# Optimization experiments

Measured on AMD Instinct MI355X. Metric: run time of the kernel, lower is better.

Reference implementation:

```python
import jax, jax.numpy as jnp
import numpy as np

D_MODEL = 1024
N_HEADS = 16
HEAD_DIM = D_MODEL // N_HEADS  # 64
BASE = 10000.0
MAX_X, MAX_Y, MAX_Z = 32, 32, 8
NEG_INF = -1e9  # stand-in for float('-inf') in masked_fill; identical after softmax


def _split_dims(head_dim):
    n_pairs = head_dim // 2
    px = n_pairs // 3
    py = n_pairs // 3
    pz = n_pairs - px - py
    return px * 2, py * 2, pz * 2


def _cos_sin_table(dim, max_pos):
    # matches RotaryEmbedding3D._register_cache
    inv_freq = 1.0 / (BASE ** (np.arange(0, dim, 2, dtype=np.float32) / dim))
    t = np.arange(max_pos, dtype=np.float32)[:, None] * inv_freq  # [max_pos, dim/2]
    cos = np.repeat(np.cos(t), 2, axis=-1)  # repeat_interleave(2)
    sin = np.repeat(np.sin(t), 2, axis=-1)
    return jnp.asarray(cos), jnp.asarray(sin)


def _rotate_half(x):
    x1 = x[..., ::2]
    x2 = x[..., 1::2]
    return jnp.stack((-x2, x1), axis=-1).reshape(x.shape)


def setup_inputs() -> dict:
    key = jax.random.key(0)
    k1, k2, k3, k4, k5, k6 = jax.random.split(key, 6)
    B, S = 2, 2048
    hidden_states = jax.random.normal(k1, (B, S, D_MODEL), dtype=jnp.float32)
    w_qkv = jax.random.normal(k2, (D_MODEL, 3 * D_MODEL), dtype=jnp.float32) * 0.02
    w_out = jax.random.normal(k3, (D_MODEL, D_MODEL), dtype=jnp.float32) * 0.02
    px = jax.random.randint(k4, (B, S, 1), 0, MAX_X)
    py = jax.random.randint(k5, (B, S, 1), 0, MAX_Y)
    pz = jax.random.randint(k6, (B, S, 1), 0, MAX_Z)
    pos_xyz = jnp.concatenate([px, py, pz], axis=-1).astype(jnp.int64)
    causal_mask = jnp.triu(jnp.ones((S, S), dtype=bool), k=1)[None, None]  # [1,1,S,S]
    return {"hidden_states": hidden_states, "w_qkv": w_qkv, "w_out": w_out,
            "pos_xyz": pos_xyz, "causal_mask": causal_mask}


def reference(hidden_states, w_qkv, w_out, pos_xyz, causal_mask):
    B, S, D = hidden_states.shape
    H, Hd = N_HEADS, HEAD_DIM
    # fused QKV projection
    qkv = hidden_states @ w_qkv  # [B,S,3D]
    qkv = qkv.reshape(B, S, 3, H, Hd).transpose(2, 0, 3, 1, 4)  # [3,B,H,S,Hd]
    q, k, v = qkv[0], qkv[1], qkv[2]
    # 3D RoPE tables and lookups
    dx, dy, dz = _split_dims(Hd)
    cx, sx = _cos_sin_table(dx, MAX_X)
    cy, sy = _cos_sin_table(dy, MAX_Y)
    cz, sz = _cos_sin_table(dz, MAX_Z)
    ix = jnp.clip(pos_xyz[..., 0], 0, MAX_X - 1)
    iy = jnp.clip(pos_xyz[..., 1], 0, MAX_Y - 1)
    iz = jnp.clip(pos_xyz[..., 2], 0, MAX_Z - 1)
    cos = jnp.concatenate([cx[ix], cy[iy], cz[iz]], axis=-1)[:, None]  # [B,1,S,Hd]
    sin = jnp.concatenate([sx[ix], sy[iy], sz[iz]], axis=-1)[:, None]
    q = q * cos + _rotate_half(q) * sin
    k = k * cos + _rotate_half(k) * sin
    # SDPA with causal bias
    scale = Hd ** -0.5
    scores = jnp.einsum('bhqd,bhkd->bhqk', q, k) * scale
    scores = jnp.where(causal_mask, jnp.asarray(NEG_INF, scores.dtype), scores)
    probs = jax.nn.softmax(scores, axis=-1)
    attn = jnp.einsum('bhqk,bhkd->bhqd', probs, v)
    attn = attn.transpose(0, 2, 1, 3).reshape(B, S, D)
    return attn @ w_out
```

## Files before the change

### kernel.cpp

```cpp
#include <hip/hip_runtime.h>
#include <hip/hip_bf16.h>
#include <math.h>

typedef __bf16 bf16;
typedef __bf16 bf16x8 __attribute__((ext_vector_type(8)));
typedef float f32x4 __attribute__((ext_vector_type(4)));

#define SEQ 2048
#define NHEADS 16
#define HDIM 64
#define DM 1024
#define QKVW 3072

__device__ __forceinline__ void gload_lds16(const void* g, void* l) {
  __builtin_amdgcn_global_load_lds(
      (const __attribute__((address_space(1))) unsigned int*)g,
      (__attribute__((address_space(3))) unsigned int*)l, 16, 0, 0);
}

template <int CTRL>
__device__ __forceinline__ float dppmovf(float x) {
  return __builtin_bit_cast(
      float, __builtin_amdgcn_mov_dpp(__builtin_bit_cast(int, x), CTRL, 0xf,
                                      0xf, true));
}
__device__ __forceinline__ float rowsum16(float x) {
  x += dppmovf<0xB1>(x);
  x += dppmovf<0x4E>(x);
  x += dppmovf<0x124>(x);
  x += dppmovf<0x128>(x);
  return x;
}

__global__ __launch_bounds__(256) void prep(
    const float* __restrict__ hidden, const float* __restrict__ w_qkv,
    const float* __restrict__ w_out, const int* __restrict__ pos,
    bf16* __restrict__ hid_bf, bf16* __restrict__ wqkvT,
    bf16* __restrict__ woutT, float2* __restrict__ tbl) {
  __shared__ float tile[64][65];
  int idx = blockIdx.x, tid = threadIdx.x;
  if (idx < 2048) {
    int i = (idx * 256 + tid) * 8;
    float4 a = *(const float4*)(hidden + i);
    float4 b = *(const float4*)(hidden + i + 4);
    bf16x8 o;
    o[0] = (bf16)a.x; o[1] = (bf16)a.y; o[2] = (bf16)a.z; o[3] = (bf16)a.w;
    o[4] = (bf16)b.x; o[5] = (bf16)b.y; o[6] = (bf16)b.z; o[7] = (bf16)b.w;
    *(bf16x8*)(hid_bf + i) = o;
  } else if (idx < 3072) {
    const float* in; bf16* out; int R, C, t;
    if (idx < 2816) { t = idx - 2048; in = w_qkv; out = wqkvT; R = 1024; C = 3072; }
    else            { t = idx - 2816; in = w_out; out = woutT; R = 1024; C = 1024; }
    int nbx = C >> 6;
    int c0 = (t % nbx) * 64, r0 = (t / nbx) * 64;
    int col = tid & 63, rb = (tid >> 6) * 16;
#pragma unroll
    for (int i = 0; i < 16; ++i)
      tile[rb + i][col] = in[(size_t)(r0 + rb + i) * C + c0 + col];
    __syncthreads();
#pragma unroll
    for (int i = 0; i < 16; ++i)
      out[(size_t)(c0 + rb + i) * R + r0 + col] = (bf16)tile[col][rb + i];
  } else {
    const float LN1E4 = 9.210340371976184f;
    int gi = (idx - 3072) * 256 + tid;
    int m = gi >> 5, pr = gi & 31;
    int axis, d, iloc;
    if (pr < 10)      { axis = 0; d = 20; iloc = pr; }
    else if (pr < 20) { axis = 1; d = 20; iloc = pr - 10; }
    else              { axis = 2; d = 24; iloc = pr - 20; }
    int p = pos[m * 3 + axis];
    int pmax = (axis == 2) ? 7 : 31;
    p = p < 0 ? 0 : (p > pmax ? pmax : p);
    float invf = __expf(-((float)(2 * iloc) / (float)d) * LN1E4);
    float sn, cs;
    __sincosf((float)p * invf, &sn, &cs);
    tbl[gi] = make_float2(cs, sn);
  }
}

__global__ __launch_bounds__(256) void post_qkv(
    bf16* __restrict__ qkv, const float2* __restrict__ tbl,
    bf16* __restrict__ vT) {
  __shared__ bf16 btile[64][65];
  int idx = blockIdx.x, tid = threadIdx.x;
  if (idx < 2048) {
    int gi = idx * 256 + tid;
    int m = gi >> 7, seg = gi & 127;
    bf16* p = qkv + (size_t)m * QKVW + seg * 16;
    bf16x8 a = *(const bf16x8*)p;
    bf16x8 b2 = *(const bf16x8*)(p + 8);
    const float2* t = tbl + m * 32 + (((seg * 16) & 63) >> 1);
#pragma unroll
    for (int j = 0; j < 4; ++j) {
      float2 cs = t[j];
      float e = (float)a[2 * j], o = (float)a[2 * j + 1];
      a[2 * j]     = (bf16)(e * cs.x - o * cs.y);
      a[2 * j + 1] = (bf16)(o * cs.x + e * cs.y);
    }
#pragma unroll
    for (int j = 0; j < 4; ++j) {
      float2 cs = t[4 + j];
      float e = (float)b2[2 * j], o = (float)b2[2 * j + 1];
      b2[2 * j]     = (bf16)(e * cs.x - o * cs.y);
      b2[2 * j + 1] = (bf16)(o * cs.x + e * cs.y);
    }
    *(bf16x8*)p = a;
    *(bf16x8*)(p + 8) = b2;
  } else {
    int t = idx - 2048;
    int s0 = (t & 31) * 64, bh = t >> 5;
    int b = bh >> 4, h = bh & 15;
    const bf16* src = qkv + (size_t)(b * SEQ + s0) * QKVW + 2 * DM + h * 64;
    int col = tid & 63, rb = (tid >> 6) * 16;
#pragma unroll
    for (int i = 0; i < 16; ++i)
      btile[rb + i][col] = src[(size_t)(rb + i) * QKVW + col];
    __syncthreads();
    bf16* dst = vT + (size_t)bh * HDIM * SEQ + s0;
#pragma unroll
    for (int i = 0; i < 16; ++i)
      dst[(size_t)(rb + i) * SEQ + col] = btile[col][rb + i];
  }
}

template <int OUTBF>
__global__ __launch_bounds__(256) void gemm_bt(
    const bf16* __restrict__ A, const bf16* __restrict__ Bt, void* Cv,
    int M, int N, int K) {
  __shared__ __align__(16) bf16 a_lds[128 * 32];
  __shared__ __align__(16) bf16 b_lds[128 * 32];
  int tid = threadIdx.x;
  int wave = tid >> 6, lane = tid & 63;
  int quad = lane >> 4, l15 = lane & 15;
  int wm = wave >> 1, wn = wave & 1;

  int flat = blockIdx.y * gridDim.x + blockIdx.x;
  int mband = gridDim.y >> 3;
  int xcd = flat & 7, sidx = flat >> 3;
  int m0 = (xcd * mband + (sidx % mband)) * 128;
  int n0 = (sidx / mband) * 128;

  f32x4 acc[4][4] = {};

  for (int kt = 0; kt < K; kt += 32) {
    __syncthreads();
#pragma unroll
    for (int call = 0; call < 2; ++call) {
      int chunk = call * 256 + tid;
      int row = chunk >> 2, cc = (chunk & 3) * 8;
      gload_lds16(A + (size_t)(m0 + row) * K + kt + cc,
                  (char*)a_lds + call * 4096 + wave * 1024);
      gload_lds16(Bt + (size_t)(n0 + row) * K + kt + cc,
                  (char*)b_lds + call * 4096 + wave * 1024);
    }
    __syncthreads();
    bf16x8 af[4], bfr[4];
#pragma unroll
    for (int i = 0; i < 4; ++i) {
      af[i]  = *(const bf16x8*)(a_lds + (wm * 64 + i * 16 + l15) * 32 + quad * 8);
      bfr[i] = *(const bf16x8*)(b_lds + (wn * 64 + i * 16 + l15) * 32 + quad * 8);
    }
#pragma unroll
    for (int mi = 0; mi < 4; ++mi)
#pragma unroll
      for (int ni = 0; ni < 4; ++ni)
        acc[mi][ni] = __builtin_amdgcn_mfma_f32_16x16x32_bf16(
            af[mi], bfr[ni], acc[mi][ni], 0, 0, 0);
  }

#pragma unroll
  for (int mi = 0; mi < 4; ++mi) {
    int mb = m0 + wm * 64 + mi * 16 + quad * 4;
#pragma unroll
    for (int ni = 0; ni < 4; ++ni) {
      int n = n0 + wn * 64 + ni * 16 + l15;
#pragma unroll
      for (int r = 0; r < 4; ++r) {
        if (OUTBF)
          ((bf16*)Cv)[(size_t)(mb + r) * N + n] = (bf16)acc[mi][ni][r];
        else
          ((float*)Cv)[(size_t)(mb + r) * N + n] = acc[mi][ni][r];
      }
    }
  }
}

__global__ __launch_bounds__(256) void attn_fwd(
    const bf16* __restrict__ QKV, const bf16* __restrict__ VT,
    bf16* __restrict__ O) {
  __shared__ __align__(16) bf16 k_lds[64 * 72];
  __shared__ __align__(16) bf16 v_lds[64 * 72];
  __shared__ __align__(16) bf16 p_lds[4][16 * 80];
  const float C2 = 0.18033688011112042f;
  const float C3 = -5.770780163555854f;
  int tid = threadIdx.x;
  int wave = tid >> 6, lane = tid & 63;
  int quad = lane >> 4, l15 = lane & 15;
  int idx = blockIdx.x;
  int bh = idx & 31;
  int g = idx >> 5;
  int qt = (g < 16) ? (31 - g) : (g - 16);
  int q0 = qt * 64;
  int b = bh >> 4, h = bh & 15;
  const bf16* Qb = QKV + (size_t)b * SEQ * QKVW + h * 64;
  const bf16* Kb = Qb + DM;
  const bf16* VTb = VT + (size_t)bh * HDIM * SEQ;
  bf16* pw = p_lds[wave];

  const bf16* qr = Qb + (size_t)(q0 + wave * 16 + l15) * QKVW;
  bf16x8 qf0 = *(const bf16x8*)(qr + quad * 8);
  bf16x8 qf1 = *(const bf16x8*)(qr + 32 + quad * 8);

  int r0c = tid >> 3, off0 = (tid & 7) * 8;
  int r1c = r0c + 32;

  int niter = qt + 1;
  f32x4 o_acc[4] = {};
  float lsum[4] = {};
  int qrow[4];
#pragma unroll
  for (int r = 0; r < 4; ++r) qrow[r] = q0 + wave * 16 + quad * 4 + r;

  bf16x8 kpre0, kpre1, vpre0, vpre1;
  kpre0 = *(const bf16x8*)(Kb + (size_t)r0c * QKVW + off0);
  kpre1 = *(const bf16x8*)(Kb + (size_t)r1c * QKVW + off0);
  vpre0 = *(const bf16x8*)(VTb + (size_t)r0c * SEQ + off0);
  vpre1 = *(const bf16x8*)(VTb + (size_t)r1c * SEQ + off0);

  for (int tkv = 0; tkv < niter; ++tkv) {
    int kv0 = tkv * 64;
    __syncthreads();
    *(bf16x8*)(k_lds + r0c * 72 + off0) = kpre0;
    *(bf16x8*)(k_lds + r1c * 72 + off0) = kpre1;
    *(bf16x8*)(v_lds + r0c * 72 + off0) = vpre0;
    *(bf16x8*)(v_lds + r1c * 72 + off0) = vpre1;
    __syncthreads();
    if (tkv + 1 < niter) {
      int kn = kv0 + 64;
      kpre0 = *(const bf16x8*)(Kb + (size_t)(kn + r0c) * QKVW + off0);
      kpre1 = *(const bf16x8*)(Kb + (size_t)(kn + r1c) * QKVW + off0);
      vpre0 = *(const bf16x8*)(VTb + (size_t)r0c * SEQ + kn + off0);
      vpre1 = *(const bf16x8*)(VTb + (size_t)r1c * SEQ + kn + off0);
    }
    f32x4 s_acc[4];
#pragma unroll
    for (int nt = 0; nt < 4; ++nt) {
      const bf16* kr = k_lds + (nt * 16 + l15) * 72;
      bf16x8 kf0 = *(const bf16x8*)(kr + quad * 8);
      bf16x8 kf1 = *(const bf16x8*)(kr + 32 + quad * 8);
      f32x4 z = {};
      z = __builtin_amdgcn_mfma_f32_16x16x32_bf16(qf0, kf0, z, 0, 0, 0);
      z = __builtin_amdgcn_mfma_f32_16x16x32_bf16(qf1, kf1, z, 0, 0, 0);
      s_acc[nt] = z;
    }
    bool diag = (tkv == qt);
#pragma unroll
    for (int r = 0; r < 4; ++r) {
#pragma unroll
      for (int nt = 0; nt < 4; ++nt) {
        float p = __builtin_amdgcn_exp2f(s_acc[nt][r] * C2 + C3);
        if (diag && (kv0 + nt * 16 + l15 > qrow[r])) p = 0.f;
        lsum[r] += p;
        pw[(quad * 4 + r) * 80 + nt * 16 + l15] = (bf16)p;
      }
    }
    __asm__ volatile("s_waitcnt lgkmcnt(0)" ::: "memory");
    bf16x8 pf0 = *(const bf16x8*)(pw + l15 * 80 + quad * 8);
    bf16x8 pf1 = *(const bf16x8*)(pw + l15 * 80 + 32 + quad * 8);
#pragma unroll
    for (int nt = 0; nt < 4; ++nt) {
      const bf16* vr = v_lds + (nt * 16 + l15) * 72;
      bf16x8 vf0 = *(const bf16x8*)(vr + quad * 8);
      bf16x8 vf1 = *(const bf16x8*)(vr + 32 + quad * 8);
      o_acc[nt] = __builtin_amdgcn_mfma_f32_16x16x32_bf16(pf0, vf0, o_acc[nt], 0, 0, 0);
      o_acc[nt] = __builtin_amdgcn_mfma_f32_16x16x32_bf16(pf1, vf1, o_acc[nt], 0, 0, 0);
    }
  }
#pragma unroll
  for (int r = 0; r < 4; ++r) {
    float inv = 1.f / rowsum16(lsum[r]);
    int sq = qrow[r];
#pragma unroll
    for (int nt = 0; nt < 4; ++nt)
      O[((size_t)(b * SEQ + sq)) * DM + h * HDIM + nt * 16 + l15] =
          (bf16)(o_acc[nt][r] * inv);
  }
}

extern "C" void kernel_launch(void* const* d_in, const int* in_sizes, int n_in,
                              void* d_out, int out_size, void* d_ws,
                              size_t ws_size, hipStream_t stream) {
  const float* hidden = (const float*)d_in[0];
  const float* w_qkv  = (const float*)d_in[1];
  const float* w_out  = (const float*)d_in[2];
  const int*   pos    = (const int*)d_in[3];
  float* out = (float*)d_out;

  char* ws = (char*)d_ws;
  bf16* wqkvT  = (bf16*)ws;  ws += (size_t)3072 * 1024 * 2;
  bf16* woutT  = (bf16*)ws;  ws += (size_t)1024 * 1024 * 2;
  bf16* hid_bf = (bf16*)ws;  ws += (size_t)4096 * 1024 * 2;
  bf16* qkv_ws = (bf16*)ws;  ws += (size_t)4096 * 3072 * 2;
  bf16* vT_ws  = (bf16*)ws;  ws += (size_t)32 * SEQ * HDIM * 2;
  float2* ropetbl = (float2*)ws;
  bf16* attn_ws = hid_bf;

  prep<<<dim3(3584), 256, 0, stream>>>(hidden, w_qkv, w_out, pos,
                                       hid_bf, wqkvT, woutT, ropetbl);
  gemm_bt<1><<<dim3(24, 32), 256, 0, stream>>>(
      hid_bf, wqkvT, qkv_ws, 4096, 3072, 1024);
  post_qkv<<<dim3(3072), 256, 0, stream>>>(qkv_ws, ropetbl, vT_ws);
  attn_fwd<<<dim3(1024), 256, 0, stream>>>(qkv_ws, vT_ws, attn_ws);
  gemm_bt<0><<<dim3(8, 32), 256, 0, stream>>>(
      attn_ws, woutT, out, 4096, 1024, 1024);
}
```

Baseline: 205.6 us.

## Use 128-row query tiles with 8 waves and double-buffered K/V LDS

The attention kernel now processes 128 query rows per block with 512 threads (8 waves), so each K/V tile loaded into LDS serves twice as many query rows. The K/V LDS buffers are double-buffered, which removes one of the two barriers per iteration. The P scratch row stride changes from 80 to 72. In exchange the grid shrinks to 512 blocks, which gives coarser causal load balance, and the diagonal tiles now do more masked work.

```diff
diff --git a/kernel.cpp b/kernel.cpp
--- a/kernel.cpp
+++ b/kernel.cpp
@@ -186,12 +186,12 @@
   }
 }
 
-__global__ __launch_bounds__(256) void attn_fwd(
+__global__ __launch_bounds__(512) void attn_fwd(
     const bf16* __restrict__ QKV, const bf16* __restrict__ VT,
     bf16* __restrict__ O) {
-  __shared__ __align__(16) bf16 k_lds[64 * 72];
-  __shared__ __align__(16) bf16 v_lds[64 * 72];
-  __shared__ __align__(16) bf16 p_lds[4][16 * 80];
+  __shared__ __align__(16) bf16 k_lds[2][64 * 72];
+  __shared__ __align__(16) bf16 v_lds[2][64 * 72];
+  __shared__ __align__(16) bf16 p_lds[8][16 * 72];
   const float C2 = 0.18033688011112042f;
   const float C3 = -5.770780163555854f;
   int tid = threadIdx.x;
@@ -200,8 +200,8 @@
   int idx = blockIdx.x;
   int bh = idx & 31;
   int g = idx >> 5;
-  int qt = (g < 16) ? (31 - g) : (g - 16);
-  int q0 = qt * 64;
+  int qt2 = (g < 8) ? (15 - g) : (g - 8);
+  int q0 = qt2 * 128;
   int b = bh >> 4, h = bh & 15;
   const bf16* Qb = QKV + (size_t)b * SEQ * QKVW + h * 64;
   const bf16* Kb = Qb + DM;
@@ -213,40 +213,33 @@
   bf16x8 qf1 = *(const bf16x8*)(qr + 32 + quad * 8);
 
   int r0c = tid >> 3, off0 = (tid & 7) * 8;
-  int r1c = r0c + 32;
-
-  int niter = qt + 1;
+
+  int niter = 2 * qt2 + 2;
   f32x4 o_acc[4] = {};
   float lsum[4] = {};
   int qrow[4];
 #pragma unroll
   for (int r = 0; r < 4; ++r) qrow[r] = q0 + wave * 16 + quad * 4 + r;
 
-  bf16x8 kpre0, kpre1, vpre0, vpre1;
-  kpre0 = *(const bf16x8*)(Kb + (size_t)r0c * QKVW + off0);
-  kpre1 = *(const bf16x8*)(Kb + (size_t)r1c * QKVW + off0);
-  vpre0 = *(const bf16x8*)(VTb + (size_t)r0c * SEQ + off0);
-  vpre1 = *(const bf16x8*)(VTb + (size_t)r1c * SEQ + off0);
+  bf16x8 kpre = *(const bf16x8*)(Kb + (size_t)r0c * QKVW + off0);
+  bf16x8 vpre = *(const bf16x8*)(VTb + (size_t)r0c * SEQ + off0);
 
   for (int tkv = 0; tkv < niter; ++tkv) {
     int kv0 = tkv * 64;
-    __syncthreads();
-    *(bf16x8*)(k_lds + r0c * 72 + off0) = kpre0;
-    *(bf16x8*)(k_lds + r1c * 72 + off0) = kpre1;
-    *(bf16x8*)(v_lds + r0c * 72 + off0) = vpre0;
-    *(bf16x8*)(v_lds + r1c * 72 + off0) = vpre1;
+    bf16* kb = k_lds[tkv & 1];
+    bf16* vb = v_lds[tkv & 1];
+    *(bf16x8*)(kb + r0c * 72 + off0) = kpre;
+    *(bf16x8*)(vb + r0c * 72 + off0) = vpre;
     __syncthreads();
     if (tkv + 1 < niter) {
       int kn = kv0 + 64;
-      kpre0 = *(const bf16x8*)(Kb + (size_t)(kn + r0c) * QKVW + off0);
-      kpre1 = *(const bf16x8*)(Kb + (size_t)(kn + r1c) * QKVW + off0);
-      vpre0 = *(const bf16x8*)(VTb + (size_t)r0c * SEQ + kn + off0);
-      vpre1 = *(const bf16x8*)(VTb + (size_t)r1c * SEQ + kn + off0);
+      kpre = *(const bf16x8*)(Kb + (size_t)(kn + r0c) * QKVW + off0);
+      vpre = *(const bf16x8*)(VTb + (size_t)r0c * SEQ + kn + off0);
     }
     f32x4 s_acc[4];
 #pragma unroll
     for (int nt = 0; nt < 4; ++nt) {
-      const bf16* kr = k_lds + (nt * 16 + l15) * 72;
+      const bf16* kr = kb + (nt * 16 + l15) * 72;
       bf16x8 kf0 = *(const bf16x8*)(kr + quad * 8);
       bf16x8 kf1 = *(const bf16x8*)(kr + 32 + quad * 8);
       f32x4 z = {};
@@ -254,7 +247,7 @@
       z = __builtin_amdgcn_mfma_f32_16x16x32_bf16(qf1, kf1, z, 0, 0, 0);
       s_acc[nt] = z;
     }
-    bool diag = (tkv == qt);
+    bool diag = (tkv >= 2 * qt2);
 #pragma unroll
     for (int r = 0; r < 4; ++r) {
 #pragma unroll
@@ -262,15 +255,15 @@
         float p = __builtin_amdgcn_exp2f(s_acc[nt][r] * C2 + C3);
         if (diag && (kv0 + nt * 16 + l15 > qrow[r])) p = 0.f;
         lsum[r] += p;
-        pw[(quad * 4 + r) * 80 + nt * 16 + l15] = (bf16)p;
+        pw[(quad * 4 + r) * 72 + nt * 16 + l15] = (bf16)p;
       }
     }
     __asm__ volatile("s_waitcnt lgkmcnt(0)" ::: "memory");
-    bf16x8 pf0 = *(const bf16x8*)(pw + l15 * 80 + quad * 8);
-    bf16x8 pf1 = *(const bf16x8*)(pw + l15 * 80 + 32 + quad * 8);
+    bf16x8 pf0 = *(const bf16x8*)(pw + l15 * 72 + quad * 8);
+    bf16x8 pf1 = *(const bf16x8*)(pw + l15 * 72 + 32 + quad * 8);
 #pragma unroll
     for (int nt = 0; nt < 4; ++nt) {
-      const bf16* vr = v_lds + (nt * 16 + l15) * 72;
+      const bf16* vr = vb + (nt * 16 + l15) * 72;
       bf16x8 vf0 = *(const bf16x8*)(vr + quad * 8);
       bf16x8 vf1 = *(const bf16x8*)(vr + 32 + quad * 8);
       o_acc[nt] = __builtin_amdgcn_mfma_f32_16x16x32_bf16(pf0, vf0, o_acc[nt], 0, 0, 0);
@@ -311,7 +304,7 @@
   gemm_bt<1><<<dim3(24, 32), 256, 0, stream>>>(
       hid_bf, wqkvT, qkv_ws, 4096, 3072, 1024);
   post_qkv<<<dim3(3072), 256, 0, stream>>>(qkv_ws, ropetbl, vT_ws);
-  attn_fwd<<<dim3(1024), 256, 0, stream>>>(qkv_ws, vT_ws, attn_ws);
+  attn_fwd<<<dim3(512), 512, 0, stream>>>(qkv_ws, vT_ws, attn_ws);
   gemm_bt<0><<<dim3(8, 32), 256, 0, stream>>>(
       attn_ws, woutT, out, 4096, 1024, 1024);
 }
```

After: 204.4 us. About the same (-0.6%).
